# Kernel optimization log

Measured on AMD Instinct MI355X. Metric: run time of the kernel, lower is better.

Reference implementation:

```python
import jax, jax.numpy as jnp
import numpy as np

C = 256
HEADS = 8
HD = C // HEADS
SCALE = HD ** -0.5


def conv1x1(x, W, b):
    # x: [B,C_in,H,W], W: [C_out,C_in], b: [C_out]
    return jnp.einsum('oc,bchw->bohw', W, x) + b[None, :, None, None]


def setup_inputs() -> dict:
    key = jax.random.key(0)
    ks = jax.random.split(key, 12)
    B, H, Wd = 2, 48, 48
    s = C ** -0.5
    return {
        'x': jax.random.normal(ks[0], (B, C, H, Wd), jnp.float32),
        'uncertainty': jax.random.uniform(ks[1], (B, 1, H, Wd), jnp.float32),
        'Wq': jax.random.normal(ks[2], (C, C), jnp.float32) * s,
        'bq': jnp.zeros((C,), jnp.float32),
        'Wk': jax.random.normal(ks[3], (C, C), jnp.float32) * s,
        'bk': jnp.zeros((C,), jnp.float32),
        'Wv': jax.random.normal(ks[4], (C, C), jnp.float32) * s,
        'bv': jnp.zeros((C,), jnp.float32),
        'Wg': jax.random.normal(ks[5], (C, 1), jnp.float32),
        'bg': jnp.zeros((C,), jnp.float32),
        'Wo': jax.random.normal(ks[6], (C, C), jnp.float32) * s,
        'bo': jnp.zeros((C,), jnp.float32),
    }


def reference(x, uncertainty, Wq, bq, Wk, bk, Wv, bv, Wg, bg, Wo, bo):
    B, _, H, Wd = x.shape
    N = H * Wd
    # uncertainty gate (1x1 conv from 1 channel to C channels)
    uw = conv1x1(uncertainty, Wg, bg)            # [B,C,H,W]
    gated_x = x * (1.0 - uw)
    q = conv1x1(gated_x, Wq, bq).reshape(B, HEADS, HD, N)
    k = conv1x1(gated_x, Wk, bk).reshape(B, HEADS, HD, N)
    v = conv1x1(x, Wv, bv).reshape(B, HEADS, HD, N)
    # scores: [B,h,N,N] (query tokens n, key tokens m)
    scores = jnp.einsum('bhdn,bhdm->bhnm', q, k) * SCALE
    u_flat = uncertainty.reshape(B, 1, 1, N)      # mask over key axis
    scores = scores * (1.0 - u_flat)
    attn = jax.nn.softmax(scores, axis=-1)
    out = jnp.einsum('bhnm,bhdm->bhdn', attn, v)  # [B,h,hd,N]
    out = out.reshape(B, C, H, Wd)
    out = conv1x1(out, Wo, bo)
    return out + x
```

## Files before the change

### kernel.cpp

```cpp
#include <hip/hip_runtime.h>
#include <hip/hip_bf16.h>

typedef float f32x4 __attribute__((ext_vector_type(4)));
typedef __bf16 bf16x8 __attribute__((ext_vector_type(8)));
typedef __bf16 bf16x4 __attribute__((ext_vector_type(4)));
typedef short s16x4 __attribute__((ext_vector_type(4)));

constexpr int C = 256;
constexpr int N = 2304;
constexpr int T = 2 * N;

#if __has_builtin(__builtin_amdgcn_exp2f)
#define EXP2F(x) __builtin_amdgcn_exp2f(x)
#else
#define EXP2F(x) exp2f(x)
#endif

__device__ __forceinline__ bf16x8 load_bf8(const __bf16* p) {
    return *reinterpret_cast<const bf16x8*>(p);
}

__device__ __forceinline__ f32x4 mfma32(bf16x8 a, bf16x8 b, f32x4 c) {
    return __builtin_amdgcn_mfma_f32_16x16x32_bf16(a, b, c, 0, 0, 0);
}

#if __has_builtin(__builtin_amdgcn_mfma_f32_16x16x16bf16_1k)
__device__ __forceinline__ f32x4 mfma16(bf16x4 a, bf16x4 b, f32x4 c) {
    return __builtin_amdgcn_mfma_f32_16x16x16bf16_1k(
        __builtin_bit_cast(s16x4, a), __builtin_bit_cast(s16x4, b), c, 0, 0, 0);
}
#else
__device__ __forceinline__ f32x4 mfma16(bf16x4 a, bf16x4 b, f32x4 c) {
    f32x4 d;
    asm volatile("v_mfma_f32_16x16x16_bf16 %0, %1, %2, %3"
                 : "=v"(d) : "v"(a), "v"(b), "v"(c));
    return d;
}
#endif

__device__ __forceinline__ void gload_lds16(const __bf16* g, __bf16* l) {
    __builtin_amdgcn_global_load_lds(
        (const __attribute__((address_space(1))) void*)g,
        (__attribute__((address_space(3))) void*)l, 16, 0, 0);
}

#define VMCNT2() asm volatile("s_waitcnt vmcnt(2)" ::: "memory")
#define VMCNT0() asm volatile("s_waitcnt vmcnt(0)" ::: "memory")
#define LGKM0()  asm volatile("s_waitcnt lgkmcnt(0)" ::: "memory")

__global__ void wconv_kernel(const float* __restrict__ Wq, const float* __restrict__ Wk,
                             const float* __restrict__ Wv, const float* __restrict__ Wo,
                             __bf16* __restrict__ Wb) {
    const float* srcs[4] = {Wq, Wk, Wv, Wo};
    int m = blockIdx.x >> 6;
    int idx = (blockIdx.x & 63) * 256 + threadIdx.x;
    float4 v = reinterpret_cast<const float4*>(srcs[m])[idx];
    bf16x4 o = { (__bf16)v.x, (__bf16)v.y, (__bf16)v.z, (__bf16)v.w };
    reinterpret_cast<bf16x4*>(Wb + m * 65536)[idx] = o;
}

__global__ void prep_kernel(const float* __restrict__ x, const float* __restrict__ u,
                            const float* __restrict__ Wg, const float* __restrict__ bg,
                            __bf16* __restrict__ xT, __bf16* __restrict__ gxT) {
    __shared__ float tile[32][65];
    int b = blockIdx.z, c0 = blockIdx.y * 32, n0 = blockIdx.x * 64;
    int t = threadIdx.x;
    const float* xp = x + (b * C + c0) * N + n0;
    #pragma unroll
    for (int r = 0; r < 8; ++r) {
        int cl = r * 4 + (t >> 6);
        int nl = t & 63;
        tile[cl][nl] = xp[cl * N + nl];
    }
    __syncthreads();
    int cq = (t & 7) * 4;
    #pragma unroll
    for (int it = 0; it < 2; ++it) {
        int nl = it * 32 + (t >> 3);
        float uv = u[b * N + n0 + nl];
        bf16x4 xo, go;
        #pragma unroll
        for (int j = 0; j < 4; ++j) {
            int c = c0 + cq + j;
            float xv = tile[cq + j][nl];
            float gate = 1.0f - (Wg[c] * uv + bg[c]);
            xo[j] = (__bf16)xv;
            go[j] = (__bf16)(xv * gate);
        }
        int tok = b * N + n0 + nl;
        *reinterpret_cast<bf16x4*>(xT + (long)tok * C + c0 + cq) = xo;
        *reinterpret_cast<bf16x4*>(gxT + (long)tok * C + c0 + cq) = go;
    }
}

__global__ __launch_bounds__(256) void qkv_kernel(const __bf16* __restrict__ Wb,
    const __bf16* __restrict__ xT, const __bf16* __restrict__ gxT,
    const float* __restrict__ bq, const float* __restrict__ bk, const float* __restrict__ bv,
    const float* __restrict__ u,
    __bf16* __restrict__ Q, __bf16* __restrict__ K, __bf16* __restrict__ V) {
    int proj = blockIdx.z;
    int o0 = blockIdx.y * 64;
    int t0 = blockIdx.x * 32;
    int wave = threadIdx.x >> 6, lane = threadIdx.x & 63;
    int g = lane >> 4, r = lane & 15;
    int ow = o0 + wave * 16;
    const __bf16* W = Wb + proj * 65536;
    const __bf16* inp = (proj == 2) ? xT : gxT;
    f32x4 acc[2] = {};
    for (int k = 0; k < 8; ++k) {
        bf16x8 a = load_bf8(W + (ow + r) * C + k * 32 + g * 8);
        #pragma unroll
        for (int tb = 0; tb < 2; ++tb) {
            bf16x8 bfr = load_bf8(inp + (long)(t0 + tb * 16 + r) * C + k * 32 + g * 8);
            acc[tb] = mfma32(a, bfr, acc[tb]);
        }
    }
    const float* bias = (proj == 0) ? bq : (proj == 1) ? bk : bv;
    float bvw[4];
    #pragma unroll
    for (int i = 0; i < 4; ++i) bvw[i] = bias[ow + g * 4 + i];
    int h = ow >> 5, d0 = (ow & 31) + g * 4;
    const float SC = 0.17677669529663687f * 1.4426950408889634f;
    #pragma unroll
    for (int tb = 0; tb < 2; ++tb) {
        int t = t0 + tb * 16 + r;
        int b = t / N, n = t % N;
        if (proj == 2) {
            #pragma unroll
            for (int i = 0; i < 4; ++i)
                V[((long)(b * 8 + h) * 32 + d0 + i) * N + n] = (__bf16)(acc[tb][i] + bvw[i]);
        } else {
            bf16x4 outv;
            if (proj == 1) {
                float scale = SC * (1.0f - u[t]);
                #pragma unroll
                for (int i = 0; i < 4; ++i) outv[i] = (__bf16)((acc[tb][i] + bvw[i]) * scale);
            } else {
                #pragma unroll
                for (int i = 0; i < 4; ++i) outv[i] = (__bf16)(acc[tb][i] + bvw[i]);
            }
            __bf16* dst = (proj == 0) ? Q : K;
            *reinterpret_cast<bf16x4*>(dst + ((long)(b * 8 + h) * N + n) * 32 + d0) = outv;
        }
    }
}

__global__ __launch_bounds__(256) void attn_kernel(const __bf16* __restrict__ Q,
    const __bf16* __restrict__ K, const __bf16* __restrict__ V,
    __bf16* __restrict__ aoT) {
    __shared__ __bf16 sK[2][2048];
    __shared__ __bf16 sV[2][2048];
    int id = blockIdx.x;
    int xcd = id & 7, j = id >> 3;
    int bh = xcd + 8 * (j / 36);
    int qblk = j % 36;
    int tid = threadIdx.x;
    int wave = tid >> 6, lane = tid & 63;
    int g = lane >> 4, r = lane & 15;
    int q0w = qblk * 64 + wave * 16;
    const __bf16* Qg = Q + (long)bh * N * 32;
    const __bf16* Kg = K + (long)bh * N * 32;
    const __bf16* Vg = V + (long)bh * 32 * N;
    bf16x8 qf = load_bf8(Qg + (q0w + r) * 32 + g * 8);
    int l_ = tid ^ ((tid >> 3) & 7);
    const __bf16* kS = Kg + (l_ >> 2) * 32 + (l_ & 3) * 8;
    const __bf16* vS = Vg + (long)(l_ >> 3) * N + (l_ & 7) * 8;
    int so = wave * 512;
    auto STAGE = [&](long m0, __bf16* kd, __bf16* vd) {
        gload_lds16(kS + m0 * 32, kd + so);
        gload_lds16(vS + m0,      vd + so);
    };
    int pk[4], pv[4][2];
    #pragma unroll
    for (int t = 0; t < 4; ++t) {
        int ck = (t * 16 + r) * 4 + g;
        pk[t] = (ck ^ ((ck >> 3) & 7)) * 8;
        #pragma unroll
        for (int dt = 0; dt < 2; ++dt) {
            int cv = (dt * 16 + r) * 8 + t * 2 + (g >> 1);
            pv[t][dt] = (cv ^ ((cv >> 3) & 7)) * 8 + (g & 1) * 4;
        }
    }
    bf16x4 onesv;
    #pragma unroll
    for (int i = 0; i < 4; ++i) onesv[i] = (__bf16)1.0f;
    f32x4 oa0 = {}, oa1 = {}, oal = {};
    STAGE(0,  &sK[0][0], &sV[0][0]);
    STAGE(64, &sK[1][0], &sV[1][0]);
    for (int t = 0; t < 36; ++t) {
        if (t < 35) { VMCNT2(); } else { VMCNT0(); }
        __builtin_amdgcn_s_barrier();
        const __bf16* kb = &sK[t & 1][0];
        const __bf16* vb = &sV[t & 1][0];
        bf16x8 kc0 = load_bf8(kb + pk[0]);
        bf16x8 kc1 = load_bf8(kb + pk[1]);
        bf16x8 kc2 = load_bf8(kb + pk[2]);
        bf16x8 kc3 = load_bf8(kb + pk[3]);
        bf16x4 vf[4][2];
        #pragma unroll
        for (int tt = 0; tt < 4; ++tt)
            #pragma unroll
            for (int dt = 0; dt < 2; ++dt)
                vf[tt][dt] = *reinterpret_cast<const bf16x4*>(vb + pv[tt][dt]);
        f32x4 z = {};
        __builtin_amdgcn_s_setprio(1);
        f32x4 s0 = mfma32(kc0, qf, z);
        f32x4 s1 = mfma32(kc1, qf, z);
        f32x4 s2 = mfma32(kc2, qf, z);
        f32x4 s3 = mfma32(kc3, qf, z);
        __builtin_amdgcn_s_setprio(0);
        bf16x4 pa0, pa1, pa2, pa3;
        #pragma unroll
        for (int i = 0; i < 4; ++i) pa0[i] = (__bf16)EXP2F(s0[i]);
        #pragma unroll
        for (int i = 0; i < 4; ++i) pa1[i] = (__bf16)EXP2F(s1[i]);
        #pragma unroll
        for (int i = 0; i < 4; ++i) pa2[i] = (__bf16)EXP2F(s2[i]);
        #pragma unroll
        for (int i = 0; i < 4; ++i) pa3[i] = (__bf16)EXP2F(s3[i]);
        __builtin_amdgcn_s_setprio(1);
        oa0 = mfma16(vf[0][0], pa0, oa0);
        oa1 = mfma16(vf[0][1], pa0, oa1);
        oal = mfma16(onesv,    pa0, oal);
        oa0 = mfma16(vf[1][0], pa1, oa0);
        oa1 = mfma16(vf[1][1], pa1, oa1);
        oal = mfma16(onesv,    pa1, oal);
        oa0 = mfma16(vf[2][0], pa2, oa0);
        oa1 = mfma16(vf[2][1], pa2, oa1);
        oal = mfma16(onesv,    pa2, oal);
        oa0 = mfma16(vf[3][0], pa3, oa0);
        oa1 = mfma16(vf[3][1], pa3, oa1);
        oal = mfma16(onesv,    pa3, oal);
        __builtin_amdgcn_s_setprio(0);
        LGKM0();
        __builtin_amdgcn_s_barrier();
        if (t < 34)
            STAGE((long)(t + 2) * 64, &sK[t & 1][0], &sV[t & 1][0]);
    }
    float inv = 1.0f / oal[0];
    int b = bh >> 3, h = bh & 7;
    long tok = (long)b * N + q0w + r;
    bf16x4 ov0, ov1;
    #pragma unroll
    for (int i = 0; i < 4; ++i) ov0[i] = (__bf16)(oa0[i] * inv);
    #pragma unroll
    for (int i = 0; i < 4; ++i) ov1[i] = (__bf16)(oa1[i] * inv);
    *reinterpret_cast<bf16x4*>(aoT + tok * C + h * 32 + g * 4) = ov0;
    *reinterpret_cast<bf16x4*>(aoT + tok * C + h * 32 + 16 + g * 4) = ov1;
}

__global__ __launch_bounds__(256) void outp_kernel(const __bf16* __restrict__ Wb,
    const __bf16* __restrict__ aoT, const float* __restrict__ bo,
    const float* __restrict__ x, float* __restrict__ out) {
    int o0 = blockIdx.y * 64;
    int t0 = blockIdx.x * 16;
    int wave = threadIdx.x >> 6, lane = threadIdx.x & 63;
    int g = lane >> 4, r = lane & 15;
    int ow = o0 + wave * 16;
    const __bf16* W = Wb + 3 * 65536;
    f32x4 acc = {};
    for (int k = 0; k < 8; ++k) {
        bf16x8 a = load_bf8(W + (ow + r) * C + k * 32 + g * 8);
        bf16x8 bfr = load_bf8(aoT + (long)(t0 + r) * C + k * 32 + g * 8);
        acc = mfma32(a, bfr, acc);
    }
    float bvw[4];
    #pragma unroll
    for (int i = 0; i < 4; ++i) bvw[i] = bo[ow + g * 4 + i];
    int t = t0 + r;
    int b = t / N, n = t % N;
    #pragma unroll
    for (int i = 0; i < 4; ++i) {
        long idx = ((long)b * C + ow + g * 4 + i) * N + n;
        out[idx] = acc[i] + bvw[i] + x[idx];
    }
}

extern "C" void kernel_launch(void* const* d_in, const int* in_sizes, int n_in,
                              void* d_out, int out_size, void* d_ws, size_t ws_size,
                              hipStream_t stream) {
    const float* x  = (const float*)d_in[0];
    const float* u  = (const float*)d_in[1];
    const float* Wq = (const float*)d_in[2];
    const float* bq = (const float*)d_in[3];
    const float* Wk = (const float*)d_in[4];
    const float* bk = (const float*)d_in[5];
    const float* Wv = (const float*)d_in[6];
    const float* bv = (const float*)d_in[7];
    const float* Wg = (const float*)d_in[8];
    const float* bg = (const float*)d_in[9];
    const float* Wo = (const float*)d_in[10];
    const float* bo = (const float*)d_in[11];
    float* out = (float*)d_out;

    char* ws = (char*)d_ws;
    size_t off = 0;
    auto alloc = [&](size_t bytes) {
        char* p = ws + off;
        off += (bytes + 255) & ~(size_t)255;
        return p;
    };
    __bf16* Wb  = (__bf16*)alloc((size_t)4 * 65536 * 2);
    __bf16* xT  = (__bf16*)alloc((size_t)T * C * 2);
    __bf16* gxT = (__bf16*)alloc((size_t)T * C * 2);
    __bf16* Qb  = (__bf16*)alloc((size_t)16 * N * 32 * 2);
    __bf16* Kb  = (__bf16*)alloc((size_t)16 * N * 32 * 2);
    __bf16* Vb  = (__bf16*)alloc((size_t)16 * N * 32 * 2);
    __bf16* aoT = (__bf16*)alloc((size_t)T * C * 2);

    wconv_kernel<<<256, 256, 0, stream>>>(Wq, Wk, Wv, Wo, Wb);
    prep_kernel<<<dim3(36, 8, 2), 256, 0, stream>>>(x, u, Wg, bg, xT, gxT);
    qkv_kernel<<<dim3(144, 4, 3), 256, 0, stream>>>(Wb, xT, gxT, bq, bk, bv, u, Qb, Kb, Vb);
    attn_kernel<<<576, 256, 0, stream>>>(Qb, Kb, Vb, aoT);
    outp_kernel<<<dim3(288, 4), 256, 0, stream>>>(Wb, aoT, bo, x, out);
}
```

Before: 81.40 us.

## Fold weight conversion into prep kernel and retile QKV projection blocks

The separate weight-to-bf16 conversion kernel is merged into the prep kernel as extra blocks, removing one kernel launch. The QKV projection is retiled so each block covers one head's 32 output channels across 128 tokens, with each wave computing four 16-token tiles instead of two. This halves the grid size and lets each A-fragment load feed more MFMAs. The block index is also reordered so the head sits in the low bits. Launch overhead and redundant weight loads should drop, at the cost of more accumulator registers per wave and fewer blocks.

New measurement: 76.42 us. 6.1% less time.

```diff
diff --git a/kernel.cpp b/kernel.cpp
--- a/kernel.cpp
+++ b/kernel.cpp
@@ -48,27 +48,32 @@
 #define VMCNT0() asm volatile("s_waitcnt vmcnt(0)" ::: "memory")
 #define LGKM0()  asm volatile("s_waitcnt lgkmcnt(0)" ::: "memory")
 
-__global__ void wconv_kernel(const float* __restrict__ Wq, const float* __restrict__ Wk,
-                             const float* __restrict__ Wv, const float* __restrict__ Wo,
-                             __bf16* __restrict__ Wb) {
-    const float* srcs[4] = {Wq, Wk, Wv, Wo};
-    int m = blockIdx.x >> 6;
-    int idx = (blockIdx.x & 63) * 256 + threadIdx.x;
-    float4 v = reinterpret_cast<const float4*>(srcs[m])[idx];
-    bf16x4 o = { (__bf16)v.x, (__bf16)v.y, (__bf16)v.z, (__bf16)v.w };
-    reinterpret_cast<bf16x4*>(Wb + m * 65536)[idx] = o;
-}
-
 __global__ void prep_kernel(const float* __restrict__ x, const float* __restrict__ u,
                             const float* __restrict__ Wg, const float* __restrict__ bg,
-                            __bf16* __restrict__ xT, __bf16* __restrict__ gxT) {
+                            const float* __restrict__ Wq, const float* __restrict__ Wk,
+                            const float* __restrict__ Wv, const float* __restrict__ Wo,
+                            __bf16* __restrict__ xT, __bf16* __restrict__ gxT,
+                            __bf16* __restrict__ Wb) {
     __shared__ float tile[32][65];
-    int b = blockIdx.z, c0 = blockIdx.y * 32, n0 = blockIdx.x * 64;
     int t = threadIdx.x;
+    if (blockIdx.x >= 576) {
+        int u2 = blockIdx.x - 576;
+        const float* srcs[4] = {Wq, Wk, Wv, Wo};
+        int m = u2 >> 6;
+        int idx = (u2 & 63) * 256 + t;
+        float4 v = reinterpret_cast<const float4*>(srcs[m])[idx];
+        bf16x4 o = { (__bf16)v.x, (__bf16)v.y, (__bf16)v.z, (__bf16)v.w };
+        reinterpret_cast<bf16x4*>(Wb + m * 65536)[idx] = o;
+        return;
+    }
+    int uu = blockIdx.x;
+    int n0 = (uu % 36) * 64;
+    int c0 = ((uu / 36) & 7) * 32;
+    int b = uu / 288;
     const float* xp = x + (b * C + c0) * N + n0;
     #pragma unroll
-    for (int r = 0; r < 8; ++r) {
-        int cl = r * 4 + (t >> 6);
+    for (int rr = 0; rr < 8; ++rr) {
+        int cl = rr * 4 + (t >> 6);
         int nl = t & 63;
         tile[cl][nl] = xp[cl * N + nl];
     }
@@ -80,12 +85,12 @@
         float uv = u[b * N + n0 + nl];
         bf16x4 xo, go;
         #pragma unroll
-        for (int j = 0; j < 4; ++j) {
-            int c = c0 + cq + j;
-            float xv = tile[cq + j][nl];
-            float gate = 1.0f - (Wg[c] * uv + bg[c]);
-            xo[j] = (__bf16)xv;
-            go[j] = (__bf16)(xv * gate);
+        for (int jj = 0; jj < 4; ++jj) {
+            int cch = c0 + cq + jj;
+            float xv = tile[cq + jj][nl];
+            float gate = 1.0f - (Wg[cch] * uv + bg[cch]);
+            xo[jj] = (__bf16)xv;
+            go[jj] = (__bf16)(xv * gate);
         }
         int tok = b * N + n0 + nl;
         *reinterpret_cast<bf16x4*>(xT + (long)tok * C + c0 + cq) = xo;
@@ -98,40 +103,43 @@
     const float* __restrict__ bq, const float* __restrict__ bk, const float* __restrict__ bv,
     const float* __restrict__ u,
     __bf16* __restrict__ Q, __bf16* __restrict__ K, __bf16* __restrict__ V) {
-    int proj = blockIdx.z;
-    int o0 = blockIdx.y * 64;
-    int t0 = blockIdx.x * 32;
+    int L = blockIdx.x;
+    int h = L & 7;
+    int rest = L >> 3;
+    int c = rest % 36;
+    int z = rest / 36;
     int wave = threadIdx.x >> 6, lane = threadIdx.x & 63;
     int g = lane >> 4, r = lane & 15;
-    int ow = o0 + wave * 16;
-    const __bf16* W = Wb + proj * 65536;
-    const __bf16* inp = (proj == 2) ? xT : gxT;
-    f32x4 acc[2] = {};
+    int ow = h * 32 + (wave & 1) * 16;
+    int t0 = c * 128 + (wave >> 1) * 64;
+    const __bf16* W = Wb + z * 65536;
+    const __bf16* inp = (z == 2) ? xT : gxT;
+    f32x4 acc[4] = {};
     for (int k = 0; k < 8; ++k) {
         bf16x8 a = load_bf8(W + (ow + r) * C + k * 32 + g * 8);
         #pragma unroll
-        for (int tb = 0; tb < 2; ++tb) {
+        for (int tb = 0; tb < 4; ++tb) {
             bf16x8 bfr = load_bf8(inp + (long)(t0 + tb * 16 + r) * C + k * 32 + g * 8);
             acc[tb] = mfma32(a, bfr, acc[tb]);
         }
     }
-    const float* bias = (proj == 0) ? bq : (proj == 1) ? bk : bv;
+    const float* bias = (z == 0) ? bq : (z == 1) ? bk : bv;
     float bvw[4];
     #pragma unroll
     for (int i = 0; i < 4; ++i) bvw[i] = bias[ow + g * 4 + i];
-    int h = ow >> 5, d0 = (ow & 31) + g * 4;
+    int d0 = (wave & 1) * 16 + g * 4;
     const float SC = 0.17677669529663687f * 1.4426950408889634f;
     #pragma unroll
-    for (int tb = 0; tb < 2; ++tb) {
+    for (int tb = 0; tb < 4; ++tb) {
         int t = t0 + tb * 16 + r;
         int b = t / N, n = t % N;
-        if (proj == 2) {
+        if (z == 2) {
             #pragma unroll
             for (int i = 0; i < 4; ++i)
                 V[((long)(b * 8 + h) * 32 + d0 + i) * N + n] = (__bf16)(acc[tb][i] + bvw[i]);
         } else {
             bf16x4 outv;
-            if (proj == 1) {
+            if (z == 1) {
                 float scale = SC * (1.0f - u[t]);
                 #pragma unroll
                 for (int i = 0; i < 4; ++i) outv[i] = (__bf16)((acc[tb][i] + bvw[i]) * scale);
@@ -139,7 +147,7 @@
                 #pragma unroll
                 for (int i = 0; i < 4; ++i) outv[i] = (__bf16)(acc[tb][i] + bvw[i]);
             }
-            __bf16* dst = (proj == 0) ? Q : K;
+            __bf16* dst = (z == 0) ? Q : K;
             *reinterpret_cast<bf16x4*>(dst + ((long)(b * 8 + h) * N + n) * 32 + d0) = outv;
         }
     }
@@ -308,9 +316,8 @@
     __bf16* Vb  = (__bf16*)alloc((size_t)16 * N * 32 * 2);
     __bf16* aoT = (__bf16*)alloc((size_t)T * C * 2);
 
-    wconv_kernel<<<256, 256, 0, stream>>>(Wq, Wk, Wv, Wo, Wb);
-    prep_kernel<<<dim3(36, 8, 2), 256, 0, stream>>>(x, u, Wg, bg, xT, gxT);
-    qkv_kernel<<<dim3(144, 4, 3), 256, 0, stream>>>(Wb, xT, gxT, bq, bk, bv, u, Qb, Kb, Vb);
+    prep_kernel<<<832, 256, 0, stream>>>(x, u, Wg, bg, Wq, Wk, Wv, Wo, xT, gxT, Wb);
+    qkv_kernel<<<864, 256, 0, stream>>>(Wb, xT, gxT, bq, bk, bv, u, Qb, Kb, Vb);
     attn_kernel<<<576, 256, 0, stream>>>(Qb, Kb, Vb, aoT);
     outp_kernel<<<dim3(288, 4), 256, 0, stream>>>(Wb, aoT, bo, x, out);
 }
```
